# Kernel tuning notes

Measured on AMD Instinct MI355X. Metric: run time of the kernel, lower is better.

Reference implementation:

```python
import jax, jax.numpy as jnp
import numpy as np

VOCAB = 34004
EMB = 300
UNITS = 512


def setup_inputs() -> dict:
    key = jax.random.key(0)
    ks = jax.random.split(key, 16)
    s = 0.05
    B, T_in, T_out = 64, 60, 31
    inp = {
        "dec_input": jax.random.randint(ks[0], (B, T_out), 0, VOCAB, dtype=jnp.int64 if jax.config.jax_enable_x64 else jnp.int32),
        "h0": jax.random.normal(ks[1], (B, UNITS), jnp.float32),
        "c0": jax.random.normal(ks[2], (B, UNITS), jnp.float32),
        "memory": jax.random.normal(ks[3], (B, T_in, UNITS), jnp.float32),
        # embedding table
        "embedding": jax.random.normal(ks[4], (VOCAB, EMB), jnp.float32) * s,
        # LSTM cell: input = concat(emb, prev_attention) -> EMB + UNITS
        "Wk": jax.random.normal(ks[5], (EMB + UNITS, 4 * UNITS), jnp.float32) * s,
        "Uk": jax.random.normal(ks[6], (UNITS, 4 * UNITS), jnp.float32) * s,
        "bk": jnp.zeros((4 * UNITS,), jnp.float32),
        # Bahdanau attention: memory layer, query layer, score vector v
        "Wm": jax.random.normal(ks[7], (UNITS, UNITS), jnp.float32) * s,
        "Wq": jax.random.normal(ks[8], (UNITS, UNITS), jnp.float32) * s,
        "v_att": jax.random.normal(ks[9], (UNITS,), jnp.float32) * s,
        # attention_layer (Dense(dec_units, use_bias=False)) on concat(cell_out, context)
        "Wa": jax.random.normal(ks[10], (2 * UNITS, UNITS), jnp.float32) * s,
        # output projection fc to vocab
        "Wfc": jax.random.normal(ks[11], (UNITS, VOCAB), jnp.float32) * s,
        "bfc": jnp.zeros((VOCAB,), jnp.float32),
    }
    return inp


def reference(dec_input, h0, c0, memory, embedding, Wk, Uk, bk, Wm, Wq, v_att, Wa, Wfc, bfc):
    # Teacher-forced (training=True) AttentionWrapper decode with Bahdanau attention.
    keys = jnp.einsum("btd,de->bte", memory, Wm)  # precompute memory projection [B,T_in,U]
    emb = embedding[dec_input]                      # [B,T_out,EMB]
    emb_t = jnp.swapaxes(emb, 0, 1)                 # [T_out,B,EMB]
    attn0 = jnp.zeros_like(h0)                      # initial attention is zeros

    def step(carry, e):
        h, c, attn = carry
        x = jnp.concatenate([e, attn], axis=-1)     # default cell_input_fn: concat
        z = x @ Wk + h @ Uk + bk                    # [B,4U]
        i, f, g, o = jnp.split(z, 4, axis=-1)       # keras LSTM gate order i,f,c,o
        i = jax.nn.sigmoid(i); f = jax.nn.sigmoid(f)
        g = jnp.tanh(g); o = jax.nn.sigmoid(o)
        c_new = f * c + i * g
        h_new = o * jnp.tanh(c_new)
        # Bahdanau score: v^T tanh(W_m*memory + W_q*query)
        q = h_new @ Wq                               # [B,U]
        score = jnp.einsum("btu,u->bt", jnp.tanh(keys + q[:, None, :]), v_att)
        align = jax.nn.softmax(score, axis=-1)       # [B,T_in]
        context = jnp.einsum("bt,btd->bd", align, memory)
        attn_new = jnp.concatenate([h_new, context], axis=-1) @ Wa  # attention_layer
        logits = attn_new @ Wfc + bfc                # output_layer (fc)
        return (h_new, c_new, attn_new), logits

    _, logits = jax.lax.scan(step, (h0, c0, attn0), emb_t)
    return jnp.swapaxes(logits, 0, 1)               # [B, T_out, vocab] = rnn_output
```

## Files before the change

### kernel.cpp

```cpp
#include <hip/hip_runtime.h>
#include <cstdint>
#include <cstddef>

typedef _Float16 f16;
typedef _Float16 f16x8 __attribute__((ext_vector_type(8)));
typedef _Float16 f16x2 __attribute__((ext_vector_type(2)));
typedef float    f32x4 __attribute__((ext_vector_type(4)));
typedef uint32_t u32x4 __attribute__((ext_vector_type(4)));

#define DEV static __device__ __forceinline__

constexpr int TOUT = 31;
constexpr int VOC  = 34004;
constexpr int VOCP = 34048;

constexpr size_t OFF_SYNC  = 0;
constexpr size_t OFF_MEM16 = 8192;
constexpr size_t OFF_WMSWZ = OFF_MEM16 + (size_t)3840*512*2;
constexpr size_t OFF_KEYS  = OFF_WMSWZ + (size_t)16*512*32*2;
constexpr size_t OFF_EMBA  = OFF_KEYS  + (size_t)3840*512*2;
constexpr size_t OFF_WKTOP = OFF_EMBA  + (size_t)1984*320*2;
constexpr size_t OFF_EMBW  = OFF_WKTOP + (size_t)10*2048*32*2;
constexpr size_t OFF_WA16  = OFF_EMBW  + (size_t)1984*2048*4;
constexpr size_t OFF_WKATT = OFF_WA16  + (size_t)1024*512*2;
constexpr size_t OFF_WCA   = OFF_WKATT + (size_t)16*2048*32*2;
constexpr size_t OFF_WSTAR = OFF_WCA   + (size_t)1024*2048*4;
constexpr size_t OFF_UK16  = OFF_WSTAR + (size_t)32*2048*32*2;
constexpr size_t OFF_WQSWZ = OFF_UK16  + (size_t)16*2048*32*2;
constexpr size_t OFF_WASWZ = OFF_WQSWZ + (size_t)512*512*2;
constexpr size_t OFF_H016  = OFF_WASWZ + (size_t)32*512*32*2;
constexpr size_t OFF_YALL  = OFF_H016  + (size_t)64*512*2;
constexpr size_t OFF_ATT16 = OFF_YALL  + (size_t)31*64*1024*2;
constexpr size_t OFF_BKP   = OFF_ATT16 + (size_t)1984*512*2;
constexpr size_t OFF_WFC   = OFF_BKP   + 8192;
constexpr size_t OFF_QP    = OFF_EMBA;

DEV void gload16(const void* src, void* ldsbase ) {
  __builtin_amdgcn_global_load_lds(
      (const __attribute__((address_space(1))) unsigned int*)src,
      (__attribute__((address_space(3))) unsigned int*)ldsbase, 16, 0, 0);
}

DEV float sigm(float x)      { return 1.f / (1.f + expf(-x)); }
DEV float tanh_fast(float x) { float e = __expf(2.f*x); return 1.f - 2.f/(e+1.f); }

DEV uint32_t aload_u32(const uint32_t* p){ return __hip_atomic_load(p, __ATOMIC_RELAXED, __HIP_MEMORY_SCOPE_AGENT); }
DEV void astore_u32(uint32_t* p, uint32_t v){ __hip_atomic_store(p, v, __ATOMIC_RELAXED, __HIP_MEMORY_SCOPE_AGENT); }

DEV void ld16_sc1(const void* p, u32x4& d){
  asm volatile("global_load_dwordx4 %0, %1, off sc1" : "=v"(d) : "v"(p));
}
DEV void st16_sc1(void* p, u32x4 v){
  asm volatile("global_store_dwordx4 %0, %1, off sc1" :: "v"(p), "v"(v) : "memory");
}
DEV void vwait(){ asm volatile("s_waitcnt vmcnt(0)" ::: "memory"); }

__global__ void prep_elem(char* ws, const int* dec, const float* h0,
                          const float* memory, const float* embt,
                          const float* Wa, const float* bk)
{
  f16* mem16 = (f16*)(ws+OFF_MEM16);
  f16* embA  = (f16*)(ws+OFF_EMBA);
  f16* wa16  = (f16*)(ws+OFF_WA16);
  f16* h016  = (f16*)(ws+OFF_H016);
  float* bkp = (float*)(ws+OFF_BKP);
  constexpr int E0=1966080, E1=E0+634880, E2=E1+524288, E3=E2+32768, E4=E3+2048;
  for (int i = blockIdx.x*256 + threadIdx.x; i < E4; i += gridDim.x*256) {
    if (i < E0) { mem16[i] = (f16)memory[i]; }
    else if (i < E1) { int j=i-E0; int r=j/320, k=j-r*320; int t=r>>6, b=r&63;
      int tok = dec[b*TOUT+t];
      embA[j] = (k<300) ? (f16)embt[(size_t)tok*300+k] : (f16)0.f; }
    else if (i < E2) { int j=i-E1; wa16[j] = (f16)Wa[j]; }
    else if (i < E3) { int j=i-E2; h016[j] = (f16)h0[j]; }
    else { int j=i-E3; bkp[j] = bk[(j>>2) + (j&3)*512]; }
  }
}

__global__ void prep_swz(char* ws, const float* Wm, const float* Wk, const float* Uk,
                         const float* Wa, const float* Wq)
{
  int tg = blockIdx.x*256 + threadIdx.x;
  constexpr int S0=8192, S1=S0+20480, S2=S1+32768, S3=S2+32768, S4=S3+16384, S5=S4+8192;
  if (tg >= S5) return;
  f16 buf[32];
  f16* dst;
  if (tg < S0) {
    int kt=tg>>9, n=tg&511;
    #pragma unroll
    for (int kk=0;kk<32;kk++) buf[kk] = (f16)Wm[(size_t)(kt*32+kk)*512 + n];
    dst = (f16*)(ws+OFF_WMSWZ) + (size_t)tg*32;
  } else if (tg < S1) {
    int j=tg-S0; int kt=j>>11, np=j&2047; int col=(np>>2)+(np&3)*512;
    #pragma unroll
    for (int kk=0;kk<32;kk++){ int k=kt*32+kk;
      buf[kk] = (k<300) ? (f16)Wk[(size_t)k*2048+col] : (f16)0.f; }
    dst = (f16*)(ws+OFF_WKTOP) + (size_t)j*32;
  } else if (tg < S2) {
    int j=tg-S1; int kt=j>>11, np=j&2047; int col=(np>>2)+(np&3)*512;
    #pragma unroll
    for (int kk=0;kk<32;kk++) buf[kk] = (f16)Wk[(size_t)(300+kt*32+kk)*2048+col];
    dst = (f16*)(ws+OFF_WKATT) + (size_t)j*32;
  } else if (tg < S3) {
    int j=tg-S2; int kt=j>>11, np=j&2047; int col=(np>>2)+(np&3)*512;
    #pragma unroll
    for (int kk=0;kk<32;kk++) buf[kk] = (f16)Uk[(size_t)(kt*32+kk)*2048+col];
    dst = (f16*)(ws+OFF_UK16) + (size_t)j*32;
  } else if (tg < S4) {
    int j=tg-S3; int kt=j>>9, n=j&511;
    #pragma unroll
    for (int kk=0;kk<32;kk++) buf[kk] = (f16)Wa[(size_t)(kt*32+kk)*512 + n];
    dst = (f16*)(ws+OFF_WASWZ) + (size_t)j*32;
  } else {
    int j=tg-S4; int rr=j>>9, n=j&511;
    #pragma unroll
    for (int kk=0;kk<32;kk++) buf[kk] = (f16)Wq[(size_t)(rr*32+kk)*512 + n];
    dst = (f16*)(ws+OFF_WQSWZ) + (size_t)j*32;
  }
  f16x8* d8 = (f16x8*)dst; f16x8* s8 = (f16x8*)buf;
  d8[0]=s8[0]; d8[1]=s8[1]; d8[2]=s8[2]; d8[3]=s8[3];
}

__global__ void prep_wfc(char* ws, const float* Wfc)
{
  int n  = blockIdx.x*256 + threadIdx.x;
  int kt = blockIdx.y;
  f16 buf[32];
  #pragma unroll
  for (int kk=0;kk<32;kk++)
    buf[kk] = (n < VOC) ? (f16)Wfc[(size_t)(kt*32+kk)*VOC + n] : (f16)0.f;
  f16* dst = (f16*)(ws+OFF_WFC) + ((size_t)kt*VOCP + n)*32;
  f16x8* d8 = (f16x8*)dst; f16x8* s8 = (f16x8*)buf;
  d8[0]=s8[0]; d8[1]=s8[1]; d8[2]=s8[2]; d8[3]=s8[3];
}

__global__ void build_wstar(char* ws, const float* Uk)
{
  int tg = blockIdx.x*256 + threadIdx.x;
  int kt = tg>>11, np = tg&2047;
  int col = (np>>2)+(np&3)*512;
  const float* wca = (const float*)(ws+OFF_WCA);
  f16 buf[32];
  #pragma unroll
  for (int kk=0;kk<32;kk++){
    int k = kt*32+kk;
    float v = wca[(size_t)k*2048 + np];
    if (k < 512) v += Uk[(size_t)k*2048 + col];
    buf[kk] = (f16)v;
  }
  f16* dst = (f16*)(ws+OFF_WSTAR) + (size_t)tg*32;
  f16x8* d8 = (f16x8*)dst; f16x8* s8 = (f16x8*)buf;
  d8[0]=s8[0]; d8[1]=s8[1]; d8[2]=s8[2]; d8[3]=s8[3];
}

template<int BM, int BN, int WR, int WC, int MODE>
__global__ __launch_bounds__(WR*WC*64, 1)
void gemm16(const f16* __restrict__ A, int lda,
            const f16* __restrict__ Bs, int Np,
            void* __restrict__ C, const float* __restrict__ bias,
            int M, int K, int Mreal, int Nreal)
{
  constexpr int NT  = WR*WC*64;
  constexpr int WTM = BM/WR, WTN = BN/WC, AM = WTM/16, AN = WTN/16;
  constexpr int NLA = BM*64/(NT*16), NLB = BN*64/(NT*16);
  __shared__ __align__(16) f16 sA[BM*32];
  __shared__ __align__(16) f16 sB[BN*32];
  const int tid = threadIdx.x, wave = tid>>6, lane = tid&63;
  const int lg = lane>>4, lr = lane&15;
  const int m0 = blockIdx.y*BM, n0 = blockIdx.x*BN;
  const int wm = (wave/WC)*WTM, wn = (wave%WC)*WTN;

  f32x4 acc[AM][AN] = {};

  int aoff[AM], boff[AN];
  #pragma unroll
  for (int i=0;i<AM;i++){ int row = wm+i*16+lr; aoff[i] = row*64 + (((lg + (row>>1))&3)<<4); }
  #pragma unroll
  for (int i=0;i<AN;i++){ int row = wn+i*16+lr; boff[i] = row*64 + (((lg + (row>>1))&3)<<4); }

  const int ksteps = K/32;
  for (int ks=0; ks<ksteps; ks++){
    const int k0 = ks*32;
    __syncthreads();
    #pragma unroll
    for (int i=0;i<NLA;i++){
      int p = i*NT + tid;
      int row = p>>2; int g = ((p&3) - (row>>1)) & 3;
      int gm = m0+row; if (gm > Mreal-1) gm = Mreal-1;
      gload16(A + (size_t)gm*lda + k0 + g*8, (char*)sA + (i*NT + wave*64)*16);
    }
    #pragma unroll
    for (int i=0;i<NLB;i++){
      int p = i*NT + tid;
      int row = p>>2; int g = ((p&3) - (row>>1)) & 3;
      gload16(Bs + ((size_t)(k0>>5)*Np + (n0+row))*32 + g*8, (char*)sB + (i*NT + wave*64)*16);
    }
    __syncthreads();
    f16x8 af[AM], bf[AN];
    #pragma unroll
    for (int i=0;i<AM;i++) af[i] = *(const f16x8*)((const char*)sA + aoff[i]);
    #pragma unroll
    for (int i=0;i<AN;i++) bf[i] = *(const f16x8*)((const char*)sB + boff[i]);
    #pragma unroll
    for (int i=0;i<AM;i++)
      #pragma unroll
      for (int j=0;j<AN;j++)
        acc[i][j] = __builtin_amdgcn_mfma_f32_16x16x32_f16(af[i], bf[j], acc[i][j], 0,0,0);
  }

  #pragma unroll
  for (int i=0;i<AM;i++)
    #pragma unroll
    for (int j=0;j<AN;j++){
      int n = n0 + wn + j*16 + lr;
      if (MODE == 2 && n >= Nreal) continue;
      float bb = 0.f;
      if (MODE != 1 && bias) bb = bias[n];
      #pragma unroll
      for (int r=0;r<4;r++){
        int m = m0 + wm + i*16 + lg*4 + r;
        if (m >= Mreal) continue;
        float v = acc[i][j][r] + bb;
        if (MODE == 0)      ((float*)C)[(size_t)m*Np + n] = v;
        else if (MODE == 1) ((f16*)C)[(size_t)m*Np + n] = (f16)v;
        else { int t = m>>6, b = m&63; ((float*)C)[((size_t)(b*TOUT+t))*VOC + n] = v; }
      }
    }
}

DEV void cbar(uint32_t* flags, int cbase, int r, int tid, uint32_t target)
{
  vwait();
  __syncthreads();
  if (tid == 0)
    astore_u32(flags + (size_t)(cbase + r)*32, target);
  if (tid < 16) {
    while (aload_u32(flags + (size_t)(cbase + tid)*32) < target)
      __builtin_amdgcn_s_sleep(1);
  }
  __syncthreads();
}

template<int KS>
DEV f32x4 p1_mfma(const f16* __restrict__ Bs, const char* ylb, int col, int kg, int lr)
{
  f16x8 B[8];
  #pragma unroll
  for (int i=0;i<8;i++)
    B[i] = *(const f16x8*)(Bs + (((size_t)i*2048 + col)<<5) + kg*8);
  f32x4 acc = {};
  #pragma unroll
  for (int ks=0; ks<KS; ks+=8) {
    #pragma unroll
    for (int i=0;i<8;i++) {
      f16x8 a = *(const f16x8*)(ylb + lr*2064 + (ks+i)*64 + kg*16);
      acc = __builtin_amdgcn_mfma_f32_16x16x32_f16(a, B[i], acc, 0,0,0);
      int nk = ks+8+i;
      if (nk < KS)
        B[i] = *(const f16x8*)(Bs + (((size_t)nk*2048 + col)<<5) + kg*8);
    }
  }
  return acc;
}

__global__ __launch_bounds__(512, 1)
void recur(char* ws, const float* __restrict__ c0, const float* __restrict__ v_att)
{
  const int blk = blockIdx.x, tid = threadIdx.x;
  const int wave = tid>>6, lane = tid&63;
  const int lr = lane&15, kg = lane>>4;
  const int clus = blk>>4, r = blk&15;
  const int cbase = clus<<4;
  const int bown = cbase + r;
  const int n0 = r*128;

  uint32_t* flags = (uint32_t*)(ws+OFF_SYNC);
  char* qpg = (char*)(ws+OFF_QP);
  const f16* wstar = (const f16*)(ws+OFF_WSTAR);
  const f16* uk16  = (const f16*)(ws+OFF_UK16);
  const f16* wqswz = (const f16*)(ws+OFF_WQSWZ);
  const f16* keys16= (const f16*)(ws+OFF_KEYS);
  const f16* mem16 = (const f16*)(ws+OFF_MEM16);
  const float* embw= (const float*)(ws+OFF_EMBW);

  __shared__ __align__(16) char  ybuf[33024];
  __shared__ __align__(16) float zl[16*132];
  __shared__ __align__(16) float c_sl[512];
  __shared__ __align__(16) f16   h_sl[512];
  __shared__ __align__(16) float q_l[512];
  __shared__ __align__(16) float v_l[512];
  __shared__ __align__(16) f16   cx16_l[512];
  __shared__ __align__(16) float sc_l[64];
  __shared__ __align__(16) f16   mem_lds[60*512];

  v_l[tid] = v_att[tid];
  { int b = tid>>5, uu = tid&31;
    c_sl[tid] = c0[(size_t)(cbase+b)*512 + r*32 + uu]; }

  {
    const char* msrc = (const char*)(mem16 + (size_t)bown*60*512);
    #pragma unroll
    for (int i=0;i<8;i++){
      int cb = i*512 + wave*64;
      if (cb < 3840)
        gload16(msrc + ((size_t)cb + lane)*16, (char*)mem_lds + (size_t)cb*16);
    }
  }

  for (int t=0; t<TOUT; t++){
    {
      const char* ysrc; int rsh;
      if (t == 0) { ysrc = ws+OFF_H016; rsh = 6; }
      else        { ysrc = ws+OFF_YALL + (size_t)(t-1)*64*2048; rsh = 7; }
      const int npass = (16 << rsh) >> 9;
      u32x4 g[4];
      #pragma unroll
      for (int p=0;p<4;p++){
        if (p < npass){
          int cid = p*512 + tid, row = cid>>rsh, off = cid & ((1<<rsh)-1);
          ld16_sc1(ysrc + ((size_t)(cbase+row) << (rsh+4)) + off*16, g[p]);
        }
      }
      vwait();
      #pragma unroll
      for (int p=0;p<4;p++){
        if (p < npass){
          int cid = p*512 + tid, row = cid>>rsh, off = cid & ((1<<rsh)-1);
          *(u32x4*)(ybuf + row*2064 + off*16) = g[p];
        }
      }
      __syncthreads();
    }

    {
      const int col = n0 + wave*16 + lr;
      f32x4 acc = (t==0) ? p1_mfma<16>(uk16,  ybuf, col, kg, lr)
                         : p1_mfma<32>(wstar, ybuf, col, kg, lr);
      #pragma unroll
      for (int rr=0;rr<4;rr++)
        zl[(kg*4+rr)*132 + wave*16 + lr] = acc[rr];
    }
    __syncthreads();

    {
      const int b = tid>>5, uu = tid&31;
      f32x4 zz = *(const f32x4*)(zl + b*132 + uu*4);
      f32x4 e  = *(const f32x4*)(embw + ((size_t)(t*64+cbase+b))*2048 + n0 + uu*4);
      float ig = sigm(zz[0]+e[0]), fg = sigm(zz[1]+e[1]);
      float gg = tanhf(zz[2]+e[2]), og = sigm(zz[3]+e[3]);
      float cn = fg*c_sl[tid] + ig*gg;
      c_sl[tid] = cn;
      h_sl[tid] = (f16)(og * tanhf(cn));
    }
    __syncthreads();

    char* yt = (char*)(ws+OFF_YALL) + (size_t)t*64*2048;
    if (tid < 64){
      int b = tid>>2, off = tid&3;
      u32x4 v = *(const u32x4*)((const char*)h_sl + b*64 + off*16);
      st16_sc1(yt + (size_t)(cbase+b)*2048 + r*64 + off*16, v);
    }

    {
      float* qs = (float*)ybuf;
      f16x8 a = *(const f16x8*)(h_sl + lr*32 + kg*8);
      #pragma unroll
      for (int j=0;j<4;j++){
        int n = wave*64 + j*16 + lr;
        f16x8 bf = *(const f16x8*)(wqswz + ((size_t)(r*512 + n))*32 + kg*8);
        f32x4 aq = __builtin_amdgcn_mfma_f32_16x16x32_f16(a, bf, (f32x4){0.f,0.f,0.f,0.f}, 0,0,0);
        #pragma unroll
        for (int rr=0;rr<4;rr++)
          qs[(kg*4+rr)*512 + n] = aq[rr];
      }
    }
    __syncthreads();
    {
      #pragma unroll
      for (int p=0;p<4;p++){
        int cid = p*512 + tid;
        u32x4 v = *(const u32x4*)(ybuf + cid*16);
        st16_sc1(qpg + (size_t)blk*32768 + cid*16, v);
      }
    }
    cbar(flags, cbase, r, tid, 2*t+1);

    {
      u32x4 gq[4];
      #pragma unroll
      for (int p=0;p<4;p++){
        int cid = p*512 + tid, s = cid>>7, off = cid&127;
        ld16_sc1(qpg + (size_t)(cbase+s)*32768 + r*2048 + off*16, gq[p]);
      }
      vwait();
      #pragma unroll
      for (int p=0;p<4;p++){
        int cid = p*512 + tid;
        *(u32x4*)(ybuf + cid*16) = gq[p];
      }
      __syncthreads();
      const float* qin = (const float*)ybuf;
      float qsum = 0.f;
      #pragma unroll
      for (int s=0;s<16;s++) qsum += qin[s*512 + tid];
      q_l[tid] = qsum;
    }
    __syncthreads();

    for (int i = wave; i < 60; i += 8){
      const f16* krow = keys16 + ((size_t)(bown*60+i))*512;
      float p = 0.f;
      #pragma unroll
      for (int s=0;s<8;s++){
        int u = lane + s*64;
        p += tanh_fast((float)krow[u] + q_l[u]) * v_l[u];
      }
      #pragma unroll
      for (int m=32;m;m>>=1) p += __shfl_xor(p, m, 64);
      if (lane == 0) sc_l[i] = p;
    }
    __syncthreads();
    if (wave == 0){
      float s = (lane < 60) ? sc_l[lane] : -1e30f;
      float mx = s;
      #pragma unroll
      for (int m=32;m;m>>=1) mx = fmaxf(mx, __shfl_xor(mx, m, 64));
      float ev = (lane < 60) ? __expf(s - mx) : 0.f;
      float sum = ev;
      #pragma unroll
      for (int m=32;m;m>>=1) sum += __shfl_xor(sum, m, 64);
      if (lane < 60) sc_l[lane] = ev / sum;
    }
    __syncthreads();
    {
      float cx = 0.f;
      #pragma unroll
      for (int i=0;i<60;i++) cx += sc_l[i] * (float)mem_lds[i*512 + tid];
      cx16_l[tid] = (f16)cx;
    }
    __syncthreads();
    if (tid < 64){
      u32x4 v = *(const u32x4*)((const char*)cx16_l + tid*16);
      st16_sc1(yt + (size_t)bown*2048 + 1024 + tid*16, v);
    }
    cbar(flags, cbase, r, tid, 2*t+2);
  }
}

extern "C" void kernel_launch(void* const* d_in, const int* in_sizes, int n_in,
                              void* d_out, int out_size, void* d_ws, size_t ws_size,
                              hipStream_t stream)
{
  const int*   dec  = (const int*)  d_in[0];
  const float* h0   = (const float*)d_in[1];
  const float* c0   = (const float*)d_in[2];
  const float* mem  = (const float*)d_in[3];
  const float* embt = (const float*)d_in[4];
  const float* Wk   = (const float*)d_in[5];
  const float* Uk   = (const float*)d_in[6];
  const float* bk   = (const float*)d_in[7];
  const float* Wm   = (const float*)d_in[8];
  const float* Wq   = (const float*)d_in[9];
  const float* va   = (const float*)d_in[10];
  const float* Wa   = (const float*)d_in[11];
  const float* Wfc  = (const float*)d_in[12];
  const float* bfc  = (const float*)d_in[13];
  char* ws = (char*)d_ws;

  hipMemsetAsync(ws + OFF_SYNC, 0, 8192, stream);

  prep_elem<<<4096, 256, 0, stream>>>(ws, dec, h0, mem, embt, Wa, bk);
  prep_swz <<<464, 256, 0, stream>>>(ws, Wm, Wk, Uk, Wa, Wq);
  prep_wfc <<<dim3(133,16), 256, 0, stream>>>(ws, Wfc);

  gemm16<128,64,2,2,1><<<dim3(8,30), 256, 0, stream>>>(
      (const f16*)(ws+OFF_MEM16), 512, (const f16*)(ws+OFF_WMSWZ), 512,
      ws+OFF_KEYS, nullptr, 3840, 512, 3840, 512);
  gemm16<128,64,2,2,0><<<dim3(32,16), 256, 0, stream>>>(
      (const f16*)(ws+OFF_EMBA), 320, (const f16*)(ws+OFF_WKTOP), 2048,
      ws+OFF_EMBW, (const float*)(ws+OFF_BKP), 1984, 320, 1984, 2048);
  gemm16<128,64,2,2,0><<<dim3(32,8), 256, 0, stream>>>(
      (const f16*)(ws+OFF_WA16), 512, (const f16*)(ws+OFF_WKATT), 2048,
      ws+OFF_WCA, nullptr, 1024, 512, 1024, 2048);
  build_wstar<<<256, 256, 0, stream>>>(ws, Uk);

  recur<<<64, 512, 0, stream>>>(ws, c0, va);

  gemm16<128,64,2,2,1><<<dim3(8,16), 256, 0, stream>>>(
      (const f16*)(ws+OFF_YALL), 1024, (const f16*)(ws+OFF_WASWZ), 512,
      ws+OFF_ATT16, nullptr, 1984, 1024, 1984, 512);
  gemm16<256,128,4,2,2><<<dim3(266,8), 512, 0, stream>>>(
      (const f16*)(ws+OFF_ATT16), 512, (const f16*)(ws+OFF_WFC), VOCP,
      d_out, bfc, 1984, 512, 1984, VOC);
}
```

Before: 836.6 us.

## Fuse recurrence, attention projection and vocab projection into one persistent kernel

Replaces the separate recurrence kernel, the attention-layer GEMM and the vocab-projection GEMM with a single persistent kernel of 205 blocks. 64 blocks run the LSTM/attention recurrence, 8 blocks compute each step's attention output as soon as that step's flags are set, and 133 blocks compute the vocab logits per timestep using flag polling. The Wfc fp16 swizzle moves inside the consumer blocks, so weight conversion and the output projection overlap with the serial recurrence. The cost is spin-wait polling and reliance on all 205 blocks being co-resident, since the kernel deadlocks otherwise, plus per-timestep small GEMMs that reuse weights less.

```diff
diff --git a/kernel.cpp b/kernel.cpp
--- a/kernel.cpp
+++ b/kernel.cpp
@@ -4,7 +4,6 @@
 
 typedef _Float16 f16;
 typedef _Float16 f16x8 __attribute__((ext_vector_type(8)));
-typedef _Float16 f16x2 __attribute__((ext_vector_type(2)));
 typedef float    f32x4 __attribute__((ext_vector_type(4)));
 typedef uint32_t u32x4 __attribute__((ext_vector_type(4)));
 
@@ -15,7 +14,8 @@
 constexpr int VOCP = 34048;
 
 constexpr size_t OFF_SYNC  = 0;
-constexpr size_t OFF_MEM16 = 8192;
+constexpr size_t OFF_AFLAG = 8192;
+constexpr size_t OFF_MEM16 = 16384;
 constexpr size_t OFF_WMSWZ = OFF_MEM16 + (size_t)3840*512*2;
 constexpr size_t OFF_KEYS  = OFF_WMSWZ + (size_t)16*512*32*2;
 constexpr size_t OFF_EMBA  = OFF_KEYS  + (size_t)3840*512*2;
@@ -31,8 +31,8 @@
 constexpr size_t OFF_H016  = OFF_WASWZ + (size_t)32*512*32*2;
 constexpr size_t OFF_YALL  = OFF_H016  + (size_t)64*512*2;
 constexpr size_t OFF_ATT16 = OFF_YALL  + (size_t)31*64*1024*2;
-constexpr size_t OFF_BKP   = OFF_ATT16 + (size_t)1984*512*2;
-constexpr size_t OFF_WFC   = OFF_BKP   + 8192;
+constexpr size_t OFF_BKP   = OFF_ATT16 + (size_t)31*64*512*2;
+constexpr size_t OFF_WFCS  = OFF_BKP   + 8192;
 constexpr size_t OFF_QP    = OFF_EMBA;
 
 DEV void gload16(const void* src, void* ldsbase ) {
@@ -46,6 +46,10 @@
 
 DEV uint32_t aload_u32(const uint32_t* p){ return __hip_atomic_load(p, __ATOMIC_RELAXED, __HIP_MEMORY_SCOPE_AGENT); }
 DEV void astore_u32(uint32_t* p, uint32_t v){ __hip_atomic_store(p, v, __ATOMIC_RELAXED, __HIP_MEMORY_SCOPE_AGENT); }
+
+DEV uint32_t pack16(f16 a, f16 b){
+  union { f16 h[2]; uint32_t u; } c; c.h[0]=a; c.h[1]=b; return c.u;
+}
 
 DEV void ld16_sc1(const void* p, u32x4& d){
   asm volatile("global_load_dwordx4 %0, %1, off sc1" : "=v"(d) : "v"(p));
@@ -120,19 +124,6 @@
   d8[0]=s8[0]; d8[1]=s8[1]; d8[2]=s8[2]; d8[3]=s8[3];
 }
 
-__global__ void prep_wfc(char* ws, const float* Wfc)
-{
-  int n  = blockIdx.x*256 + threadIdx.x;
-  int kt = blockIdx.y;
-  f16 buf[32];
-  #pragma unroll
-  for (int kk=0;kk<32;kk++)
-    buf[kk] = (n < VOC) ? (f16)Wfc[(size_t)(kt*32+kk)*VOC + n] : (f16)0.f;
-  f16* dst = (f16*)(ws+OFF_WFC) + ((size_t)kt*VOCP + n)*32;
-  f16x8* d8 = (f16x8*)dst; f16x8* s8 = (f16x8*)buf;
-  d8[0]=s8[0]; d8[1]=s8[1]; d8[2]=s8[2]; d8[3]=s8[3];
-}
-
 __global__ void build_wstar(char* ws, const float* Uk)
 {
   int tg = blockIdx.x*256 + threadIdx.x;
@@ -212,7 +203,6 @@
     #pragma unroll
     for (int j=0;j<AN;j++){
       int n = n0 + wn + j*16 + lr;
-      if (MODE == 2 && n >= Nreal) continue;
       float bb = 0.f;
       if (MODE != 1 && bias) bb = bias[n];
       #pragma unroll
@@ -221,8 +211,7 @@
         if (m >= Mreal) continue;
         float v = acc[i][j][r] + bb;
         if (MODE == 0)      ((float*)C)[(size_t)m*Np + n] = v;
-        else if (MODE == 1) ((f16*)C)[(size_t)m*Np + n] = (f16)v;
-        else { int t = m>>6, b = m&63; ((float*)C)[((size_t)(b*TOUT+t))*VOC + n] = v; }
+        else                ((f16*)C)[(size_t)m*Np + n] = (f16)v;
       }
     }
 }
@@ -240,13 +229,13 @@
   __syncthreads();
 }
 
-template<int KS>
+template<int KS, int NS>
 DEV f32x4 p1_mfma(const f16* __restrict__ Bs, const char* ylb, int col, int kg, int lr)
 {
   f16x8 B[8];
   #pragma unroll
   for (int i=0;i<8;i++)
-    B[i] = *(const f16x8*)(Bs + (((size_t)i*2048 + col)<<5) + kg*8);
+    B[i] = *(const f16x8*)(Bs + (((size_t)i*NS + col)<<5) + kg*8);
   f32x4 acc = {};
   #pragma unroll
   for (int ks=0; ks<KS; ks+=8) {
@@ -256,193 +245,330 @@
       acc = __builtin_amdgcn_mfma_f32_16x16x32_f16(a, B[i], acc, 0,0,0);
       int nk = ks+8+i;
       if (nk < KS)
-        B[i] = *(const f16x8*)(Bs + (((size_t)nk*2048 + col)<<5) + kg*8);
+        B[i] = *(const f16x8*)(Bs + (((size_t)nk*NS + col)<<5) + kg*8);
     }
   }
   return acc;
 }
 
 __global__ __launch_bounds__(512, 1)
-void recur(char* ws, const float* __restrict__ c0, const float* __restrict__ v_att)
-{
+void mega(char* ws, const float* __restrict__ c0, const float* __restrict__ v_att,
+          const float* __restrict__ Wfc, const float* __restrict__ bfc, float* __restrict__ out)
+{
+  __shared__ __align__(16) char smem[111360];
   const int blk = blockIdx.x, tid = threadIdx.x;
   const int wave = tid>>6, lane = tid&63;
-  const int lr = lane&15, kg = lane>>4;
-  const int clus = blk>>4, r = blk&15;
-  const int cbase = clus<<4;
-  const int bown = cbase + r;
-  const int n0 = r*128;
-
-  uint32_t* flags = (uint32_t*)(ws+OFF_SYNC);
-  char* qpg = (char*)(ws+OFF_QP);
-  const f16* wstar = (const f16*)(ws+OFF_WSTAR);
-  const f16* uk16  = (const f16*)(ws+OFF_UK16);
-  const f16* wqswz = (const f16*)(ws+OFF_WQSWZ);
-  const f16* keys16= (const f16*)(ws+OFF_KEYS);
-  const f16* mem16 = (const f16*)(ws+OFF_MEM16);
-  const float* embw= (const float*)(ws+OFF_EMBW);
-
-  __shared__ __align__(16) char  ybuf[33024];
-  __shared__ __align__(16) float zl[16*132];
-  __shared__ __align__(16) float c_sl[512];
-  __shared__ __align__(16) f16   h_sl[512];
-  __shared__ __align__(16) float q_l[512];
-  __shared__ __align__(16) float v_l[512];
-  __shared__ __align__(16) f16   cx16_l[512];
-  __shared__ __align__(16) float sc_l[64];
-  __shared__ __align__(16) f16   mem_lds[60*512];
-
-  v_l[tid] = v_att[tid];
-  { int b = tid>>5, uu = tid&31;
-    c_sl[tid] = c0[(size_t)(cbase+b)*512 + r*32 + uu]; }
-
-  {
-    const char* msrc = (const char*)(mem16 + (size_t)bown*60*512);
-    #pragma unroll
-    for (int i=0;i<8;i++){
-      int cb = i*512 + wave*64;
-      if (cb < 3840)
-        gload16(msrc + ((size_t)cb + lane)*16, (char*)mem_lds + (size_t)cb*16);
-    }
-  }
-
-  for (int t=0; t<TOUT; t++){
+  const int lr = lane&15, kg = lane>>4, lg = lane>>4;
+  uint32_t* flags  = (uint32_t*)(ws+OFF_SYNC);
+  uint32_t* aflags = (uint32_t*)(ws+OFF_AFLAG);
+
+  if (blk < 64) {
+    const int clus = blk>>4, r = blk&15;
+    const int cbase = clus<<4;
+    const int bown = cbase + r;
+    const int n0 = r*128;
+
+    char*  ybuf   = smem;
+    float* zl     = (float*)(smem+33024);
+    float* c_sl   = (float*)(smem+41472);
+    f16*   h_sl   = (f16*)  (smem+43520);
+    float* q_l    = (float*)(smem+44544);
+    float* v_l    = (float*)(smem+46592);
+    f16*   cx16_l = (f16*)  (smem+48640);
+    float* sc_l   = (float*)(smem+49664);
+    f16*   mem_lds= (f16*)  (smem+49920);
+
+    char* qpg = (char*)(ws+OFF_QP);
+    const f16* wstar = (const f16*)(ws+OFF_WSTAR);
+    const f16* uk16  = (const f16*)(ws+OFF_UK16);
+    const f16* wqswz = (const f16*)(ws+OFF_WQSWZ);
+    const f16* keys16= (const f16*)(ws+OFF_KEYS);
+    const f16* mem16 = (const f16*)(ws+OFF_MEM16);
+    const float* embw= (const float*)(ws+OFF_EMBW);
+
+    v_l[tid] = v_att[tid];
+    { int b = tid>>5, uu = tid&31;
+      c_sl[tid] = c0[(size_t)(cbase+b)*512 + r*32 + uu]; }
+
     {
-      const char* ysrc; int rsh;
-      if (t == 0) { ysrc = ws+OFF_H016; rsh = 6; }
-      else        { ysrc = ws+OFF_YALL + (size_t)(t-1)*64*2048; rsh = 7; }
-      const int npass = (16 << rsh) >> 9;
-      u32x4 g[4];
+      const char* msrc = (const char*)(mem16 + (size_t)bown*60*512);
       #pragma unroll
-      for (int p=0;p<4;p++){
-        if (p < npass){
-          int cid = p*512 + tid, row = cid>>rsh, off = cid & ((1<<rsh)-1);
-          ld16_sc1(ysrc + ((size_t)(cbase+row) << (rsh+4)) + off*16, g[p]);
-        }
-      }
-      vwait();
-      #pragma unroll
-      for (int p=0;p<4;p++){
-        if (p < npass){
-          int cid = p*512 + tid, row = cid>>rsh, off = cid & ((1<<rsh)-1);
-          *(u32x4*)(ybuf + row*2064 + off*16) = g[p];
-        }
-      }
-      __syncthreads();
-    }
-
-    {
-      const int col = n0 + wave*16 + lr;
-      f32x4 acc = (t==0) ? p1_mfma<16>(uk16,  ybuf, col, kg, lr)
-                         : p1_mfma<32>(wstar, ybuf, col, kg, lr);
-      #pragma unroll
-      for (int rr=0;rr<4;rr++)
-        zl[(kg*4+rr)*132 + wave*16 + lr] = acc[rr];
-    }
+      for (int i=0;i<8;i++){
+        int cb = i*512 + wave*64;
+        if (cb < 3840)
+          gload16(msrc + ((size_t)cb + lane)*16, (char*)mem_lds + (size_t)cb*16);
+      }
+    }
+
+    for (int t=0; t<TOUT; t++){
+      {
+        const char* ysrc; int rsh;
+        if (t == 0) { ysrc = ws+OFF_H016; rsh = 6; }
+        else        { ysrc = ws+OFF_YALL + (size_t)(t-1)*64*2048; rsh = 7; }
+        const int npass = (16 << rsh) >> 9;
+        u32x4 g[4];
+        #pragma unroll
+        for (int p=0;p<4;p++){
+          if (p < npass){
+            int cid = p*512 + tid, row = cid>>rsh, off = cid & ((1<<rsh)-1);
+            ld16_sc1(ysrc + ((size_t)(cbase+row) << (rsh+4)) + off*16, g[p]);
+          }
+        }
+        vwait();
+        #pragma unroll
+        for (int p=0;p<4;p++){
+          if (p < npass){
+            int cid = p*512 + tid, row = cid>>rsh, off = cid & ((1<<rsh)-1);
+            *(u32x4*)(ybuf + row*2064 + off*16) = g[p];
+          }
+        }
+        __syncthreads();
+      }
+
+      {
+        const int col = n0 + wave*16 + lr;
+        f32x4 acc = (t==0) ? p1_mfma<16,2048>(uk16,  ybuf, col, kg, lr)
+                           : p1_mfma<32,2048>(wstar, ybuf, col, kg, lr);
+        #pragma unroll
+        for (int rr=0;rr<4;rr++)
+          zl[(kg*4+rr)*132 + wave*16 + lr] = acc[rr];
+      }
+      __syncthreads();
+
+      {
+        const int b = tid>>5, uu = tid&31;
+        f32x4 zz = *(const f32x4*)(zl + b*132 + uu*4);
+        f32x4 e  = *(const f32x4*)(embw + ((size_t)(t*64+cbase+b))*2048 + n0 + uu*4);
+        float ig = sigm(zz[0]+e[0]), fg = sigm(zz[1]+e[1]);
+        float gg = tanhf(zz[2]+e[2]), og = sigm(zz[3]+e[3]);
+        float cn = fg*c_sl[tid] + ig*gg;
+        c_sl[tid] = cn;
+        h_sl[tid] = (f16)(og * tanhf(cn));
+      }
+      __syncthreads();
+
+      char* yt = (char*)(ws+OFF_YALL) + (size_t)t*64*2048;
+      if (tid < 64){
+        int b = tid>>2, off = tid&3;
+        u32x4 v = *(const u32x4*)((const char*)h_sl + b*64 + off*16);
+        st16_sc1(yt + (size_t)(cbase+b)*2048 + r*64 + off*16, v);
+      }
+
+      {
+        float* qs = (float*)ybuf;
+        f16x8 a = *(const f16x8*)(h_sl + lr*32 + kg*8);
+        #pragma unroll
+        for (int j=0;j<4;j++){
+          int n = wave*64 + j*16 + lr;
+          f16x8 bf = *(const f16x8*)(wqswz + ((size_t)(r*512 + n))*32 + kg*8);
+          f32x4 aq = __builtin_amdgcn_mfma_f32_16x16x32_f16(a, bf, (f32x4){0.f,0.f,0.f,0.f}, 0,0,0);
+          #pragma unroll
+          for (int rr=0;rr<4;rr++)
+            qs[(kg*4+rr)*512 + n] = aq[rr];
+        }
+      }
+      __syncthreads();
+      {
+        #pragma unroll
+        for (int p=0;p<4;p++){
+          int cid = p*512 + tid;
+          u32x4 v = *(const u32x4*)(ybuf + cid*16);
+          st16_sc1(qpg + (size_t)blk*32768 + cid*16, v);
+        }
+      }
+      cbar(flags, cbase, r, tid, 2*t+1);
+
+      {
+        u32x4 gq[4];
+        #pragma unroll
+        for (int p=0;p<4;p++){
+          int cid = p*512 + tid, s = cid>>7, off = cid&127;
+          ld16_sc1(qpg + (size_t)(cbase+s)*32768 + r*2048 + off*16, gq[p]);
+        }
+        vwait();
+        #pragma unroll
+        for (int p=0;p<4;p++){
+          int cid = p*512 + tid;
+          *(u32x4*)(ybuf + cid*16) = gq[p];
+        }
+        __syncthreads();
+        const float* qin = (const float*)ybuf;
+        float qsum = 0.f;
+        #pragma unroll
+        for (int s=0;s<16;s++) qsum += qin[s*512 + tid];
+        q_l[tid] = qsum;
+      }
+      __syncthreads();
+
+      for (int i = wave; i < 60; i += 8){
+        const f16* krow = keys16 + ((size_t)(bown*60+i))*512;
+        float p = 0.f;
+        #pragma unroll
+        for (int s=0;s<8;s++){
+          int u = lane + s*64;
+          p += tanh_fast((float)krow[u] + q_l[u]) * v_l[u];
+        }
+        #pragma unroll
+        for (int m=32;m;m>>=1) p += __shfl_xor(p, m, 64);
+        if (lane == 0) sc_l[i] = p;
+      }
+      __syncthreads();
+      if (wave == 0){
+        float s = (lane < 60) ? sc_l[lane] : -1e30f;
+        float mx = s;
+        #pragma unroll
+        for (int m=32;m;m>>=1) mx = fmaxf(mx, __shfl_xor(mx, m, 64));
+        float ev = (lane < 60) ? __expf(s - mx) : 0.f;
+        float sum = ev;
+        #pragma unroll
+        for (int m=32;m;m>>=1) sum += __shfl_xor(sum, m, 64);
+        if (lane < 60) sc_l[lane] = ev / sum;
+      }
+      __syncthreads();
+      {
+        float cx = 0.f;
+        #pragma unroll
+        for (int i=0;i<60;i++) cx += sc_l[i] * (float)mem_lds[i*512 + tid];
+        cx16_l[tid] = (f16)cx;
+      }
+      __syncthreads();
+      if (tid < 64){
+        u32x4 v = *(const u32x4*)((const char*)cx16_l + tid*16);
+        st16_sc1(yt + (size_t)bown*2048 + 1024 + tid*16, v);
+      }
+      cbar(flags, cbase, r, tid, 2*t+2);
+    }
+    return;
+  }
+
+  if (blk < 72) {
+    const int a = blk - 64;
+    const int clus = a >> 1;
+    char* ybuf  = smem;
+    f16*  attst = (f16*)(smem + 33024);
+    const f16* waswz = (const f16*)(ws+OFF_WASWZ);
+
+    for (int i = tid; i < 33024/4; i += 512) ((uint32_t*)smem)[i] = 0u;
     __syncthreads();
 
-    {
-      const int b = tid>>5, uu = tid&31;
-      f32x4 zz = *(const f32x4*)(zl + b*132 + uu*4);
-      f32x4 e  = *(const f32x4*)(embw + ((size_t)(t*64+cbase+b))*2048 + n0 + uu*4);
-      float ig = sigm(zz[0]+e[0]), fg = sigm(zz[1]+e[1]);
-      float gg = tanhf(zz[2]+e[2]), og = sigm(zz[3]+e[3]);
-      float cn = fg*c_sl[tid] + ig*gg;
-      c_sl[tid] = cn;
-      h_sl[tid] = (f16)(og * tanhf(cn));
-    }
-    __syncthreads();
-
-    char* yt = (char*)(ws+OFF_YALL) + (size_t)t*64*2048;
-    if (tid < 64){
-      int b = tid>>2, off = tid&3;
-      u32x4 v = *(const u32x4*)((const char*)h_sl + b*64 + off*16);
-      st16_sc1(yt + (size_t)(cbase+b)*2048 + r*64 + off*16, v);
-    }
-
-    {
-      float* qs = (float*)ybuf;
-      f16x8 a = *(const f16x8*)(h_sl + lr*32 + kg*8);
+    for (int t=0; t<TOUT; t++){
+      if (tid < 16)
+        while (aload_u32(flags + (size_t)(clus*16 + tid)*32) < (uint32_t)(2*t+2))
+          __builtin_amdgcn_s_sleep(2);
+      __syncthreads();
+      {
+        const char* ysrc = ws + OFF_YALL + (size_t)t*131072 + (size_t)a*8*2048;
+        u32x4 g0, g1;
+        int c0i = tid, c1i = 512 + tid;
+        ld16_sc1(ysrc + (size_t)(c0i>>7)*2048 + (c0i&127)*16, g0);
+        ld16_sc1(ysrc + (size_t)(c1i>>7)*2048 + (c1i&127)*16, g1);
+        vwait();
+        *(u32x4*)(ybuf + (c0i>>7)*2064 + (c0i&127)*16) = g0;
+        *(u32x4*)(ybuf + (c1i>>7)*2064 + (c1i&127)*16) = g1;
+      }
+      __syncthreads();
       #pragma unroll
       for (int j=0;j<4;j++){
-        int n = wave*64 + j*16 + lr;
-        f16x8 bf = *(const f16x8*)(wqswz + ((size_t)(r*512 + n))*32 + kg*8);
-        f32x4 aq = __builtin_amdgcn_mfma_f32_16x16x32_f16(a, bf, (f32x4){0.f,0.f,0.f,0.f}, 0,0,0);
-        #pragma unroll
-        for (int rr=0;rr<4;rr++)
-          qs[(kg*4+rr)*512 + n] = aq[rr];
-      }
+        int col = wave*64 + j*16 + lr;
+        f32x4 acc = p1_mfma<32,512>(waswz, ybuf, col, kg, lr);
+        #pragma unroll
+        for (int rr=0;rr<4;rr++){
+          int row = lg*4 + rr;
+          if (row < 8) attst[row*512 + col] = (f16)acc[rr];
+        }
+      }
+      __syncthreads();
+      {
+        char* dst = ws + OFF_ATT16 + (size_t)t*65536 + (size_t)a*8*1024;
+        u32x4 v = *(const u32x4*)((const char*)attst + tid*16);
+        st16_sc1(dst + tid*16, v);
+        vwait();
+      }
+      __syncthreads();
+      if (tid == 0) astore_u32(aflags + (size_t)a*32, (uint32_t)(t+1));
+    }
+    return;
+  }
+
+  {
+    const int ci = blk - 72;
+    const int n0s = ci*256;
+    f16* wscr = (f16*)(ws + OFF_WFCS + (size_t)ci*262144);
+
+    for (int j = tid; j < 32768; j += 512){
+      int u = j>>6, c4 = (j&63)*4;
+      float vv0, vv1, vv2, vv3;
+      if (n0s + 256 <= VOC) {
+        f32x4 t4 = *(const f32x4*)(Wfc + (size_t)u*VOC + n0s + c4);
+        vv0=t4[0]; vv1=t4[1]; vv2=t4[2]; vv3=t4[3];
+      } else {
+        int n = n0s + c4;
+        vv0 = (n+0 < VOC) ? Wfc[(size_t)u*VOC + n+0] : 0.f;
+        vv1 = (n+1 < VOC) ? Wfc[(size_t)u*VOC + n+1] : 0.f;
+        vv2 = (n+2 < VOC) ? Wfc[(size_t)u*VOC + n+2] : 0.f;
+        vv3 = (n+3 < VOC) ? Wfc[(size_t)u*VOC + n+3] : 0.f;
+      }
+      int kt = u>>5, kk = u&31;
+      size_t base = ((size_t)kt*256 + c4) << 5;
+      wscr[base + 0*32 + kk] = (f16)vv0;
+      wscr[base + 1*32 + kk] = (f16)vv1;
+      wscr[base + 2*32 + kk] = (f16)vv2;
+      wscr[base + 3*32 + kk] = (f16)vv3;
     }
     __syncthreads();
-    {
+
+    char* attA = smem;
+    const int rt = wave&3, ch = wave>>2;
+
+    for (int t=0; t<TOUT; t++){
+      if (tid < 8)
+        while (aload_u32(aflags + (size_t)tid*32) < (uint32_t)(t+1))
+          __builtin_amdgcn_s_sleep(8);
+      __syncthreads();
+      {
+        const char* asrc = ws + OFF_ATT16 + (size_t)t*65536;
+        u32x4 g[8];
+        #pragma unroll
+        for (int p=0;p<8;p++){
+          int cid = p*512 + tid;
+          ld16_sc1(asrc + (size_t)(cid>>6)*1024 + (cid&63)*16, g[p]);
+        }
+        vwait();
+        #pragma unroll
+        for (int p=0;p<8;p++){
+          int cid = p*512 + tid;
+          *(u32x4*)(attA + (cid>>6)*1040 + (cid&63)*16) = g[p];
+        }
+      }
+      __syncthreads();
+
+      f32x4 acc[8] = {};
+      f16x8 Bp[8];
       #pragma unroll
-      for (int p=0;p<4;p++){
-        int cid = p*512 + tid;
-        u32x4 v = *(const u32x4*)(ybuf + cid*16);
-        st16_sc1(qpg + (size_t)blk*32768 + cid*16, v);
-      }
-    }
-    cbar(flags, cbase, r, tid, 2*t+1);
-
-    {
-      u32x4 gq[4];
+      for (int j=0;j<8;j++)
+        Bp[j] = *(const f16x8*)(wscr + (((size_t)(ch*128 + j*16 + lr))<<5) + kg*8);
+      for (int ks=0; ks<16; ks++){
+        f16x8 av = *(const f16x8*)(attA + (rt*16+lr)*1040 + ks*64 + kg*16);
+        #pragma unroll
+        for (int j=0;j<8;j++){
+          acc[j] = __builtin_amdgcn_mfma_f32_16x16x32_f16(av, Bp[j], acc[j], 0,0,0);
+          if (ks < 15)
+            Bp[j] = *(const f16x8*)(wscr + (((size_t)(ks+1)*256 + ch*128 + j*16 + lr)<<5) + kg*8);
+        }
+      }
       #pragma unroll
-      for (int p=0;p<4;p++){
-        int cid = p*512 + tid, s = cid>>7, off = cid&127;
-        ld16_sc1(qpg + (size_t)(cbase+s)*32768 + r*2048 + off*16, gq[p]);
-      }
-      vwait();
-      #pragma unroll
-      for (int p=0;p<4;p++){
-        int cid = p*512 + tid;
-        *(u32x4*)(ybuf + cid*16) = gq[p];
-      }
-      __syncthreads();
-      const float* qin = (const float*)ybuf;
-      float qsum = 0.f;
-      #pragma unroll
-      for (int s=0;s<16;s++) qsum += qin[s*512 + tid];
-      q_l[tid] = qsum;
-    }
-    __syncthreads();
-
-    for (int i = wave; i < 60; i += 8){
-      const f16* krow = keys16 + ((size_t)(bown*60+i))*512;
-      float p = 0.f;
-      #pragma unroll
-      for (int s=0;s<8;s++){
-        int u = lane + s*64;
-        p += tanh_fast((float)krow[u] + q_l[u]) * v_l[u];
-      }
-      #pragma unroll
-      for (int m=32;m;m>>=1) p += __shfl_xor(p, m, 64);
-      if (lane == 0) sc_l[i] = p;
-    }
-    __syncthreads();
-    if (wave == 0){
-      float s = (lane < 60) ? sc_l[lane] : -1e30f;
-      float mx = s;
-      #pragma unroll
-      for (int m=32;m;m>>=1) mx = fmaxf(mx, __shfl_xor(mx, m, 64));
-      float ev = (lane < 60) ? __expf(s - mx) : 0.f;
-      float sum = ev;
-      #pragma unroll
-      for (int m=32;m;m>>=1) sum += __shfl_xor(sum, m, 64);
-      if (lane < 60) sc_l[lane] = ev / sum;
-    }
-    __syncthreads();
-    {
-      float cx = 0.f;
-      #pragma unroll
-      for (int i=0;i<60;i++) cx += sc_l[i] * (float)mem_lds[i*512 + tid];
-      cx16_l[tid] = (f16)cx;
-    }
-    __syncthreads();
-    if (tid < 64){
-      u32x4 v = *(const u32x4*)((const char*)cx16_l + tid*16);
-      st16_sc1(yt + (size_t)bown*2048 + 1024 + tid*16, v);
-    }
-    cbar(flags, cbase, r, tid, 2*t+2);
+      for (int j=0;j<8;j++){
+        int n = n0s + ch*128 + j*16 + lr;
+        if (n < VOC){
+          float bb = bfc[n];
+          #pragma unroll
+          for (int rr=0;rr<4;rr++){
+            int b = rt*16 + lg*4 + rr;
+            out[((size_t)(b*TOUT + t))*VOC + n] = acc[j][rr] + bb;
+          }
+        }
+      }
+    }
   }
 }
 
@@ -466,11 +592,10 @@
   const float* bfc  = (const float*)d_in[13];
   char* ws = (char*)d_ws;
 
-  hipMemsetAsync(ws + OFF_SYNC, 0, 8192, stream);
+  hipMemsetAsync(ws + OFF_SYNC, 0, 16384, stream);
 
   prep_elem<<<4096, 256, 0, stream>>>(ws, dec, h0, mem, embt, Wa, bk);
   prep_swz <<<464, 256, 0, stream>>>(ws, Wm, Wk, Uk, Wa, Wq);
-  prep_wfc <<<dim3(133,16), 256, 0, stream>>>(ws, Wfc);
 
   gemm16<128,64,2,2,1><<<dim3(8,30), 256, 0, stream>>>(
       (const f16*)(ws+OFF_MEM16), 512, (const f16*)(ws+OFF_WMSWZ), 512,
@@ -483,12 +608,5 @@
       ws+OFF_WCA, nullptr, 1024, 512, 1024, 2048);
   build_wstar<<<256, 256, 0, stream>>>(ws, Uk);
 
-  recur<<<64, 512, 0, stream>>>(ws, c0, va);
-
-  gemm16<128,64,2,2,1><<<dim3(8,16), 256, 0, stream>>>(
-      (const f16*)(ws+OFF_YALL), 1024, (const f16*)(ws+OFF_WASWZ), 512,
-      ws+OFF_ATT16, nullptr, 1984, 1024, 1984, 512);
-  gemm16<256,128,4,2,2><<<dim3(266,8), 512, 0, stream>>>(
-      (const f16*)(ws+OFF_ATT16), 512, (const f16*)(ws+OFF_WFC), VOCP,
-      d_out, bfc, 1984, 512, 1984, VOC);
-}
+  mega<<<205, 512, 0, stream>>>(ws, c0, va, Wfc, bfc, (float*)d_out);
+}
```

Result: slower. 1.928 ms (+130.5%).

## Overlap Wfc conversion with recurrence and add column-resident logits GEMM

Applied to the files above, without the earlier changes.

The fp16 conversion of Wfc moves from its own kernel into extra blocks of the recurrent kernel, so it runs on CUs the 64 recurrence blocks leave idle. A new logits kernel keeps a 128-column slab of Wfc in LDS across all row tiles and streams the attention activations, in place of the generic GEMM that reloaded Wfc tiles for every row block. The goal is to hide the weight preprocessing behind the serial recurrence and to cut repeated weight traffic in the final projection. The risk is that the extra blocks compete with the recurrence for memory bandwidth, and the new GEMM has less row parallelism per block.

```diff
diff --git a/kernel.cpp b/kernel.cpp
--- a/kernel.cpp
+++ b/kernel.cpp
@@ -4,7 +4,6 @@
 
 typedef _Float16 f16;
 typedef _Float16 f16x8 __attribute__((ext_vector_type(8)));
-typedef _Float16 f16x2 __attribute__((ext_vector_type(2)));
 typedef float    f32x4 __attribute__((ext_vector_type(4)));
 typedef uint32_t u32x4 __attribute__((ext_vector_type(4)));
 
@@ -120,19 +119,6 @@
   d8[0]=s8[0]; d8[1]=s8[1]; d8[2]=s8[2]; d8[3]=s8[3];
 }
 
-__global__ void prep_wfc(char* ws, const float* Wfc)
-{
-  int n  = blockIdx.x*256 + threadIdx.x;
-  int kt = blockIdx.y;
-  f16 buf[32];
-  #pragma unroll
-  for (int kk=0;kk<32;kk++)
-    buf[kk] = (n < VOC) ? (f16)Wfc[(size_t)(kt*32+kk)*VOC + n] : (f16)0.f;
-  f16* dst = (f16*)(ws+OFF_WFC) + ((size_t)kt*VOCP + n)*32;
-  f16x8* d8 = (f16x8*)dst; f16x8* s8 = (f16x8*)buf;
-  d8[0]=s8[0]; d8[1]=s8[1]; d8[2]=s8[2]; d8[3]=s8[3];
-}
-
 __global__ void build_wstar(char* ws, const float* Uk)
 {
   int tg = blockIdx.x*256 + threadIdx.x;
@@ -212,7 +198,6 @@
     #pragma unroll
     for (int j=0;j<AN;j++){
       int n = n0 + wn + j*16 + lr;
-      if (MODE == 2 && n >= Nreal) continue;
       float bb = 0.f;
       if (MODE != 1 && bias) bb = bias[n];
       #pragma unroll
@@ -221,8 +206,7 @@
         if (m >= Mreal) continue;
         float v = acc[i][j][r] + bb;
         if (MODE == 0)      ((float*)C)[(size_t)m*Np + n] = v;
-        else if (MODE == 1) ((f16*)C)[(size_t)m*Np + n] = (f16)v;
-        else { int t = m>>6, b = m&63; ((float*)C)[((size_t)(b*TOUT+t))*VOC + n] = v; }
+        else                ((f16*)C)[(size_t)m*Np + n] = (f16)v;
       }
     }
 }
@@ -263,9 +247,30 @@
 }
 
 __global__ __launch_bounds__(512, 1)
-void recur(char* ws, const float* __restrict__ c0, const float* __restrict__ v_att)
+void recur_wfc(char* ws, const float* __restrict__ c0, const float* __restrict__ v_att,
+               const float* __restrict__ Wfc)
 {
   const int blk = blockIdx.x, tid = threadIdx.x;
+
+  if (blk >= 64) {
+    const int cb = blk - 64;
+    const int n = cb*256 + (tid & 255);
+    const int kt0 = (tid >> 8) * 8;
+    if (n < VOCP) {
+      f16* wdst = (f16*)(ws+OFF_WFC);
+      for (int kt = kt0; kt < kt0+8; kt++) {
+        f16 buf[32];
+        #pragma unroll
+        for (int kk=0;kk<32;kk++)
+          buf[kk] = (n < VOC) ? (f16)Wfc[(size_t)(kt*32+kk)*VOC + n] : (f16)0.f;
+        f16x8* d8 = (f16x8*)((f16*)wdst + ((size_t)kt*VOCP + n)*32);
+        f16x8* s8 = (f16x8*)buf;
+        d8[0]=s8[0]; d8[1]=s8[1]; d8[2]=s8[2]; d8[3]=s8[3];
+      }
+    }
+    return;
+  }
+
   const int wave = tid>>6, lane = tid&63;
   const int lr = lane&15, kg = lane>>4;
   const int clus = blk>>4, r = blk&15;
@@ -300,9 +305,9 @@
     const char* msrc = (const char*)(mem16 + (size_t)bown*60*512);
     #pragma unroll
     for (int i=0;i<8;i++){
-      int cb = i*512 + wave*64;
-      if (cb < 3840)
-        gload16(msrc + ((size_t)cb + lane)*16, (char*)mem_lds + (size_t)cb*16);
+      int cb2 = i*512 + wave*64;
+      if (cb2 < 3840)
+        gload16(msrc + ((size_t)cb2 + lane)*16, (char*)mem_lds + (size_t)cb2*16);
     }
   }
 
@@ -443,6 +448,78 @@
       st16_sc1(yt + (size_t)bown*2048 + 1024 + tid*16, v);
     }
     cbar(flags, cbase, r, tid, 2*t+2);
+  }
+}
+
+__global__ __launch_bounds__(512, 1)
+void logits_cb(const char* ws, const float* __restrict__ bfc, float* __restrict__ out)
+{
+  __shared__ __align__(16) f16 sB[16*128*32];
+  __shared__ __align__(16) f16 sA[256*32];
+  const int tid = threadIdx.x, wave = tid>>6, lane = tid&63;
+  const int lg = lane>>4, lr = lane&15;
+  const int n0 = blockIdx.x*128;
+  const int wm = (wave>>1)*64, wn = (wave&1)*64;
+  const f16* wscr = (const f16*)(ws+OFF_WFC);
+  const f16* att  = (const f16*)(ws+OFF_ATT16);
+
+  {
+    int row = tid>>2, s = tid&3;
+    int g = (s - (row>>1)) & 3;
+    #pragma unroll 4
+    for (int kt=0; kt<16; kt++){
+      gload16(wscr + ((size_t)kt*VOCP + n0 + row)*32 + g*8,
+              (char*)sB + (kt*512 + wave*64)*16);
+    }
+  }
+  __syncthreads();
+
+  int aoff[4], boff[4];
+  #pragma unroll
+  for (int i=0;i<4;i++){ int row = wm+i*16+lr; aoff[i] = row*64 + (((lg + (row>>1))&3)<<4); }
+  #pragma unroll
+  for (int j=0;j<4;j++){ int row = wn+j*16+lr; boff[j] = row*64 + (((lg + (row>>1))&3)<<4); }
+
+  for (int mt=0; mt<8; mt++){
+    const int m0 = mt*256;
+    f32x4 acc[4][4] = {};
+    for (int ks=0; ks<16; ks++){
+      __syncthreads();
+      #pragma unroll
+      for (int i=0;i<2;i++){
+        int p = i*512 + tid;
+        int row = p>>2; int g = ((p&3) - (row>>1)) & 3;
+        int gm = m0+row; if (gm > 1983) gm = 1983;
+        gload16(att + (size_t)gm*512 + ks*32 + g*8, (char*)sA + (i*512 + wave*64)*16);
+      }
+      __syncthreads();
+      f16x8 af[4], bf[4];
+      #pragma unroll
+      for (int i=0;i<4;i++) af[i] = *(const f16x8*)((const char*)sA + aoff[i]);
+      #pragma unroll
+      for (int j=0;j<4;j++) bf[j] = *(const f16x8*)((const char*)sB + ks*8192 + boff[j]);
+      #pragma unroll
+      for (int i=0;i<4;i++)
+        #pragma unroll
+        for (int j=0;j<4;j++)
+          acc[i][j] = __builtin_amdgcn_mfma_f32_16x16x32_f16(af[i], bf[j], acc[i][j], 0,0,0);
+    }
+    #pragma unroll
+    for (int j=0;j<4;j++){
+      int n = n0 + wn + j*16 + lr;
+      if (n >= VOC) continue;
+      float bb = bfc[n];
+      #pragma unroll
+      for (int i=0;i<4;i++){
+        #pragma unroll
+        for (int rr=0;rr<4;rr++){
+          int m = m0 + wm + i*16 + lg*4 + rr;
+          if (m >= 1984) continue;
+          int t = m>>6, b = m&63;
+          out[((size_t)(b*TOUT + t))*VOC + n] = acc[i][j][rr] + bb;
+        }
+      }
+    }
   }
 }
 
@@ -470,7 +547,6 @@
 
   prep_elem<<<4096, 256, 0, stream>>>(ws, dec, h0, mem, embt, Wa, bk);
   prep_swz <<<464, 256, 0, stream>>>(ws, Wm, Wk, Uk, Wa, Wq);
-  prep_wfc <<<dim3(133,16), 256, 0, stream>>>(ws, Wfc);
 
   gemm16<128,64,2,2,1><<<dim3(8,30), 256, 0, stream>>>(
       (const f16*)(ws+OFF_MEM16), 512, (const f16*)(ws+OFF_WMSWZ), 512,
@@ -483,12 +559,10 @@
       ws+OFF_WCA, nullptr, 1024, 512, 1024, 2048);
   build_wstar<<<256, 256, 0, stream>>>(ws, Uk);
 
-  recur<<<64, 512, 0, stream>>>(ws, c0, va);
+  recur_wfc<<<204, 512, 0, stream>>>(ws, c0, va, Wfc);
 
   gemm16<128,64,2,2,1><<<dim3(8,16), 256, 0, stream>>>(
       (const f16*)(ws+OFF_YALL), 1024, (const f16*)(ws+OFF_WASWZ), 512,
       ws+OFF_ATT16, nullptr, 1984, 1024, 1984, 512);
-  gemm16<256,128,4,2,2><<<dim3(266,8), 512, 0, stream>>>(
-      (const f16*)(ws+OFF_ATT16), 512, (const f16*)(ws+OFF_WFC), VOCP,
-      d_out, bfc, 1984, 512, 1984, VOC);
-}
+  logits_cb<<<266, 512, 0, stream>>>(ws, bfc, (float*)d_out);
+}
```

Result: slower. 964.7 us (+15.3%).

## Overlap Wfc fp16 conversion with recurrent kernel using spare blocks

Applied to the files above, without the earlier changes.

Removes the separate prep_wfc launch and folds the Wfc fp32-to-fp16 swizzle into extra blocks (64..203) of the recurrent kernel, so the conversion runs on CUs left idle by the 64-block latency-bound recurrence. This hides the Wfc conversion behind the recurrence instead of running it serially beforehand. Risk: the extra blocks compete for memory bandwidth with the recurrence's per-step global sync traffic. If the recurrent blocks are not all co-resident, the flag-based spin sync could also stall.

```diff
diff --git a/kernel.cpp b/kernel.cpp
--- a/kernel.cpp
+++ b/kernel.cpp
@@ -4,7 +4,6 @@
 
 typedef _Float16 f16;
 typedef _Float16 f16x8 __attribute__((ext_vector_type(8)));
-typedef _Float16 f16x2 __attribute__((ext_vector_type(2)));
 typedef float    f32x4 __attribute__((ext_vector_type(4)));
 typedef uint32_t u32x4 __attribute__((ext_vector_type(4)));
 
@@ -120,19 +119,6 @@
   d8[0]=s8[0]; d8[1]=s8[1]; d8[2]=s8[2]; d8[3]=s8[3];
 }
 
-__global__ void prep_wfc(char* ws, const float* Wfc)
-{
-  int n  = blockIdx.x*256 + threadIdx.x;
-  int kt = blockIdx.y;
-  f16 buf[32];
-  #pragma unroll
-  for (int kk=0;kk<32;kk++)
-    buf[kk] = (n < VOC) ? (f16)Wfc[(size_t)(kt*32+kk)*VOC + n] : (f16)0.f;
-  f16* dst = (f16*)(ws+OFF_WFC) + ((size_t)kt*VOCP + n)*32;
-  f16x8* d8 = (f16x8*)dst; f16x8* s8 = (f16x8*)buf;
-  d8[0]=s8[0]; d8[1]=s8[1]; d8[2]=s8[2]; d8[3]=s8[3];
-}
-
 __global__ void build_wstar(char* ws, const float* Uk)
 {
   int tg = blockIdx.x*256 + threadIdx.x;
@@ -263,9 +249,30 @@
 }
 
 __global__ __launch_bounds__(512, 1)
-void recur(char* ws, const float* __restrict__ c0, const float* __restrict__ v_att)
+void recur_wfc(char* ws, const float* __restrict__ c0, const float* __restrict__ v_att,
+               const float* __restrict__ Wfc)
 {
   const int blk = blockIdx.x, tid = threadIdx.x;
+
+  if (blk >= 64) {
+    const int cb = blk - 64;
+    const int n = cb*256 + (tid & 255);
+    const int kt0 = (tid >> 8) * 8;
+    if (n < VOCP) {
+      f16* wdst = (f16*)(ws+OFF_WFC);
+      for (int kt = kt0; kt < kt0+8; kt++) {
+        f16 buf[32];
+        #pragma unroll
+        for (int kk=0;kk<32;kk++)
+          buf[kk] = (n < VOC) ? (f16)Wfc[(size_t)(kt*32+kk)*VOC + n] : (f16)0.f;
+        f16x8* d8 = (f16x8*)((f16*)wdst + ((size_t)kt*VOCP + n)*32);
+        f16x8* s8 = (f16x8*)buf;
+        d8[0]=s8[0]; d8[1]=s8[1]; d8[2]=s8[2]; d8[3]=s8[3];
+      }
+    }
+    return;
+  }
+
   const int wave = tid>>6, lane = tid&63;
   const int lr = lane&15, kg = lane>>4;
   const int clus = blk>>4, r = blk&15;
@@ -300,9 +307,9 @@
     const char* msrc = (const char*)(mem16 + (size_t)bown*60*512);
     #pragma unroll
     for (int i=0;i<8;i++){
-      int cb = i*512 + wave*64;
-      if (cb < 3840)
-        gload16(msrc + ((size_t)cb + lane)*16, (char*)mem_lds + (size_t)cb*16);
+      int cb2 = i*512 + wave*64;
+      if (cb2 < 3840)
+        gload16(msrc + ((size_t)cb2 + lane)*16, (char*)mem_lds + (size_t)cb2*16);
     }
   }
 
@@ -470,7 +477,6 @@
 
   prep_elem<<<4096, 256, 0, stream>>>(ws, dec, h0, mem, embt, Wa, bk);
   prep_swz <<<464, 256, 0, stream>>>(ws, Wm, Wk, Uk, Wa, Wq);
-  prep_wfc <<<dim3(133,16), 256, 0, stream>>>(ws, Wfc);
 
   gemm16<128,64,2,2,1><<<dim3(8,30), 256, 0, stream>>>(
       (const f16*)(ws+OFF_MEM16), 512, (const f16*)(ws+OFF_WMSWZ), 512,
@@ -483,7 +489,7 @@
       ws+OFF_WCA, nullptr, 1024, 512, 1024, 2048);
   build_wstar<<<256, 256, 0, stream>>>(ws, Uk);
 
-  recur<<<64, 512, 0, stream>>>(ws, c0, va);
+  recur_wfc<<<204, 512, 0, stream>>>(ws, c0, va, Wfc);
 
   gemm16<128,64,2,2,1><<<dim3(8,16), 256, 0, stream>>>(
       (const f16*)(ws+OFF_YALL), 1024, (const f16*)(ws+OFF_WASWZ), 512,
```

After: 792.6 us. -5.3%, faster.
